# Performance work log

Measured on AMD Instinct MI355X. Metric: run time of the kernel, lower is better.

Reference implementation:

```python
import jax, jax.numpy as jnp
import numpy as np

T, B, I, H = 2048, 256, 512, 512


def setup_inputs() -> dict:
    key = jax.random.key(0)
    ks = jax.random.split(key, 7)
    s = 1.0 / np.sqrt(H).astype(np.float32)
    x = jax.random.normal(ks[0], (T, B, I), dtype=jnp.float32)
    # PyTorch nn.LSTM parameter layout: gates stacked as [i, f, g, o], each HxI / HxH
    W_ih = jax.random.uniform(ks[1], (4 * H, I), jnp.float32, -s, s)
    W_hh = jax.random.uniform(ks[2], (4 * H, H), jnp.float32, -s, s)
    b_ih = jax.random.uniform(ks[3], (4 * H,), jnp.float32, -s, s)
    b_hh = jax.random.uniform(ks[4], (4 * H,), jnp.float32, -s, s)
    W_out = jax.random.uniform(ks[5], (1, H), jnp.float32, -s, s)
    b_out = jax.random.uniform(ks[6], (1,), jnp.float32, -s, s)
    return {"x": x, "W_ih": W_ih, "W_hh": W_hh, "b_ih": b_ih, "b_hh": b_hh,
            "W_out": W_out, "b_out": b_out, "future": 0}


def _lstm_outputs(x, W_ih, W_hh, b_ih, b_hh):
    # Precompute input contribution for all timesteps: [T, B, 4H]
    x_proj = jnp.einsum('tbi,gi->tbg', x, W_ih) + b_ih + b_hh
    h0 = jnp.zeros((x.shape[1], W_hh.shape[1]), dtype=x.dtype)
    c0 = jnp.zeros_like(h0)

    def step(carry, xp):
        h, c = carry
        gates = xp + h @ W_hh.T                      # [B, 4H]
        i, f, g, o = jnp.split(gates, 4, axis=-1)    # torch gate order i,f,g,o
        i = jax.nn.sigmoid(i)
        f = jax.nn.sigmoid(f)
        g = jnp.tanh(g)
        o = jax.nn.sigmoid(o)
        c = f * c + i * g
        h = o * jnp.tanh(c)
        return (h, c), h

    _, hs = jax.lax.scan(step, (h0, c0), x_proj)     # hs: [T, B, H]
    return hs


def reference(x, W_ih, W_hh, b_ih, b_hh, W_out, b_out, future):
    # future == 0 in the only runnable configuration of the original module.
    hs = _lstm_outputs(x, W_ih, W_hh, b_ih, b_hh)
    out = hs @ W_out.T + b_out                       # per-step Linear(H -> 1): [T, B, 1]
    return out
```

## Files before the change

### kernel.cpp

```cpp
#include <hip/hip_runtime.h>

#define T_STEPS 2048
#define BATCH   256
#define ISZ     512
#define HSZ     512
#define GSZ     2048
#define KSZ     1024
#define XH      1024

#define SWZ(row, col) ((col) ^ (((row) & 7) << 4))

using bf16x8 = __attribute__((ext_vector_type(8))) __bf16;
using f32x4  = __attribute__((ext_vector_type(4))) float;
using i32x4  = __attribute__((ext_vector_type(4))) int;


__device__ __forceinline__ unsigned short f2bf(float f) {
    unsigned int u = __float_as_uint(f);
    unsigned int r = (u + 0x7FFFu + ((u >> 16) & 1u)) >> 16;
    return (unsigned short)r;
}
__device__ __forceinline__ float bf2f(unsigned int bits16) {
    return __uint_as_float(bits16 << 16);
}
__device__ __forceinline__ float sigf(float x)   { return 1.0f / (1.0f + __expf(-x)); }
__device__ __forceinline__ float tanh_f(float x) { return 2.0f / (1.0f + __expf(-2.0f * x)) - 1.0f; }

__global__ void pack_weights(const float* __restrict__ Wih,
                             const float* __restrict__ Whh,
                             unsigned short* __restrict__ Wcat) {
    int gid = blockIdx.x * blockDim.x + threadIdx.x;
    int n   = gid >> 8;
    int k4  = (gid & 255) * 4;
    const float* src = (k4 < ISZ) ? (Wih + (size_t)n * ISZ + k4)
                                  : (Whh + (size_t)n * HSZ + (k4 - ISZ));
    float4 v = *(const float4*)src;
    ushort4 o;
    o.x = f2bf(v.x); o.y = f2bf(v.y); o.z = f2bf(v.z); o.w = f2bf(v.w);
    *(ushort4*)(Wcat + (size_t)n * KSZ + k4) = o;
}

__global__ void init_state(unsigned int* __restrict__ thbufs,
                           float* __restrict__ bias,
                           const float* __restrict__ b_ih, const float* __restrict__ b_hh) {
    int gid = blockIdx.x * blockDim.x + threadIdx.x;
    if (gid < 262144) thbufs[gid] = 0u;
    if (gid < GSZ)    bias[gid] = b_ih[gid] + b_hh[gid];
}

__global__ __launch_bounds__(512, 2) void lstm_persist(
    const float* __restrict__ x,
    const unsigned short* __restrict__ Wcat,
    const float* __restrict__ bias,
    const float* __restrict__ Wout,
    const float* __restrict__ bout,
    unsigned long long* thbuf0,
    unsigned long long* thbuf1,
    float* __restrict__ out)
{
    __shared__ __align__(16) char xlds0[16 * XH];
    __shared__ __align__(16) char xlds1[16 * XH];
    __shared__ __align__(16) char hlds [16 * XH];
    __shared__ float gbuf[4][16][35];
    __shared__ float obuf[4];

    const int tid  = threadIdx.x;
    const int lane = tid & 63;
    const int w    = tid >> 6;
    const int gate = w & 3;
    const bool isx = (w < 4);
    const int g    = blockIdx.x & 15;
    const int wgi  = blockIdx.x >> 4;
    const int r0   = lane & 15;
    const int hi   = lane >> 4;

    const int kb = isx ? 0 : 16;
    const int n0 = gate * HSZ + wgi * 32 + r0;
    const int n1 = n0 + 16;
    bf16x8 wf0[16], wf1[16];
    #pragma unroll
    for (int it = 0; it < 16; ++it) {
        wf0[it] = *(const bf16x8*)(Wcat + (size_t)n0 * KSZ + (kb + it) * 32 + hi * 8);
        wf1[it] = *(const bf16x8*)(Wcat + (size_t)n1 * KSZ + (kb + it) * 32 + hi * 8);
    }
    #pragma unroll
    for (int it = 0; it < 16; ++it) {
        asm volatile("" : "+v"(wf0[it]));
        asm volatile("" : "+v"(wf1[it]));
    }
    const float bv0 = bias[n0];
    const float bv1 = bias[n1];
    const float bo  = bout[0];

    const int pr = tid >> 5;
    const int pc = tid & 31;
    float cst = 0.f;

    float woA = 0.f, woB = 0.f;
    if (isx) { woA = Wout[tid * 2]; woB = Wout[tid * 2 + 1]; }

    const int prow = (w - 4) * 4 + hi;
    const unsigned long long tb0 = (unsigned long long)thbuf0;
    const unsigned long long tb1 = (unsigned long long)thbuf1;
    const unsigned long long poff =
        ((unsigned long long)(g * 16 + (isx ? 0 : prow)) * 256) * 8 + (unsigned)(r0 * 16);
    const unsigned long long soff =
        ((unsigned long long)(g * 16 + pr) * 256 + wgi * 16 + (pc >> 1)) * 8;

    const int xorv = (r0 & 7) << 4;

    float4 xr[8];
    const int xrow = w * 4 + hi;
    const int xwoff = SWZ(xrow, r0 * 8);

    if (isx) {
        const float* xb = x + ((size_t)(g * 16 + xrow)) * ISZ + r0 * 4;
        #pragma unroll
        for (int s = 0; s < 8; ++s) xr[s] = *(const float4*)(xb + s * 64);
        #pragma unroll
        for (int s = 0; s < 8; ++s) {
            float4 v = xr[s];
            ushort4 o;
            o.x = f2bf(v.x); o.y = f2bf(v.y); o.z = f2bf(v.z); o.w = f2bf(v.w);
            *(ushort4*)(xlds0 + xrow * XH + xwoff + s * 128) = o;
        }
        const float* xb1 = x + ((size_t)BATCH + g * 16 + xrow) * ISZ + r0 * 4;
        #pragma unroll
        for (int s = 0; s < 8; ++s) xr[s] = *(const float4*)(xb1 + s * 64);
    }
    __syncthreads();

    #pragma unroll 1
    for (int t = 0; ; ++t) {
        if (isx) {
            if (t < T_STEPS) {
                f32x4 a0a = {0.f,0.f,0.f,0.f}, a0b = {0.f,0.f,0.f,0.f};
                f32x4 a1a = {0.f,0.f,0.f,0.f}, a1b = {0.f,0.f,0.f,0.f};
                const char* xsrc = ((t & 1) ? xlds1 : xlds0) + r0 * XH;
                #pragma unroll
                for (int it = 0; it < 16; it += 2) {
                    bf16x8 ae = *(const bf16x8*)(xsrc + ((hi * 16 + it * 64) ^ xorv));
                    bf16x8 ao = *(const bf16x8*)(xsrc + ((hi * 16 + (it + 1) * 64) ^ xorv));
                    a0a = __builtin_amdgcn_mfma_f32_16x16x32_bf16(ae, wf0[it],   a0a, 0, 0, 0);
                    a1a = __builtin_amdgcn_mfma_f32_16x16x32_bf16(ae, wf1[it],   a1a, 0, 0, 0);
                    a0b = __builtin_amdgcn_mfma_f32_16x16x32_bf16(ao, wf0[it+1], a0b, 0, 0, 0);
                    a1b = __builtin_amdgcn_mfma_f32_16x16x32_bf16(ao, wf1[it+1], a1b, 0, 0, 0);
                }
                #pragma unroll
                for (int j = 0; j < 4; ++j) {
                    gbuf[gate][hi * 4 + j][r0]      = a0a[j] + a0b[j] + bv0;
                    gbuf[gate][hi * 4 + j][16 + r0] = a1a[j] + a1b[j] + bv1;
                }
                if (t + 1 < T_STEPS) {
                    char* xd = (((t + 1) & 1) ? xlds1 : xlds0) + xrow * XH + xwoff;
                    #pragma unroll
                    for (int s = 0; s < 8; ++s) {
                        float4 v = xr[s];
                        ushort4 o;
                        o.x = f2bf(v.x); o.y = f2bf(v.y); o.z = f2bf(v.z); o.w = f2bf(v.w);
                        *(ushort4*)(xd + s * 128) = o;
                    }
                    int tp = (t + 2 < T_STEPS) ? t + 2 : T_STEPS - 1;
                    const float* xb = x + ((size_t)tp * BATCH + g * 16 + xrow) * ISZ + r0 * 4;
                    #pragma unroll
                    for (int s = 0; s < 8; ++s) xr[s] = *(const float4*)(xb + s * 64);
                }
            }
        } else {
            char* hd = hlds + prow * XH + (SWZ(prow, r0 * 8));
            if (t == 0) {
                #pragma unroll
                for (int s = 0; s < 8; ++s)
                    *(unsigned long long*)(hd + s * 128) = 0ull;
            } else {
                const unsigned long long psrc = (((t - 1) & 1) ? tb1 : tb0) + poff;
                const int tgt = t;
                i32x4 q0, q1, q2, q3, q4, q5, q6, q7;
                while (true) {
                    asm volatile(
                        "global_load_dwordx4 %0, %8, off sc0 sc1\n\t"
                        "global_load_dwordx4 %1, %8, off offset:256 sc0 sc1\n\t"
                        "global_load_dwordx4 %2, %8, off offset:512 sc0 sc1\n\t"
                        "global_load_dwordx4 %3, %8, off offset:768 sc0 sc1\n\t"
                        "global_load_dwordx4 %4, %8, off offset:1024 sc0 sc1\n\t"
                        "global_load_dwordx4 %5, %8, off offset:1280 sc0 sc1\n\t"
                        "global_load_dwordx4 %6, %8, off offset:1536 sc0 sc1\n\t"
                        "global_load_dwordx4 %7, %8, off offset:1792 sc0 sc1\n\t"
                        "s_waitcnt vmcnt(0)"
                        : "=&v"(q0), "=&v"(q1), "=&v"(q2), "=&v"(q3),
                          "=&v"(q4), "=&v"(q5), "=&v"(q6), "=&v"(q7)
                        : "v"(psrc) : "memory");
                    bool ok = (q0[1] >= tgt) & (q0[3] >= tgt) & (q1[1] >= tgt) & (q1[3] >= tgt)
                            & (q2[1] >= tgt) & (q2[3] >= tgt) & (q3[1] >= tgt) & (q3[3] >= tgt)
                            & (q4[1] >= tgt) & (q4[3] >= tgt) & (q5[1] >= tgt) & (q5[3] >= tgt)
                            & (q6[1] >= tgt) & (q6[3] >= tgt) & (q7[1] >= tgt) & (q7[3] >= tgt);
                    if (__all((int)ok)) {
                        *(unsigned long long*)(hd +   0) = (unsigned long long)(unsigned)q0[0] | ((unsigned long long)(unsigned)q0[2] << 32);
                        *(unsigned long long*)(hd + 128) = (unsigned long long)(unsigned)q1[0] | ((unsigned long long)(unsigned)q1[2] << 32);
                        *(unsigned long long*)(hd + 256) = (unsigned long long)(unsigned)q2[0] | ((unsigned long long)(unsigned)q2[2] << 32);
                        *(unsigned long long*)(hd + 384) = (unsigned long long)(unsigned)q3[0] | ((unsigned long long)(unsigned)q3[2] << 32);
                        *(unsigned long long*)(hd + 512) = (unsigned long long)(unsigned)q4[0] | ((unsigned long long)(unsigned)q4[2] << 32);
                        *(unsigned long long*)(hd + 640) = (unsigned long long)(unsigned)q5[0] | ((unsigned long long)(unsigned)q5[2] << 32);
                        *(unsigned long long*)(hd + 768) = (unsigned long long)(unsigned)q6[0] | ((unsigned long long)(unsigned)q6[2] << 32);
                        *(unsigned long long*)(hd + 896) = (unsigned long long)(unsigned)q7[0] | ((unsigned long long)(unsigned)q7[2] << 32);
                        break;
                    }
                }
            }
        }
        __syncthreads();

        if (isx) {
            if (t > 0) {
                unsigned pw2 = *(const unsigned*)(hlds + wgi * XH + (SWZ(wgi, tid * 4)));
                float ps = woA * bf2f(pw2 & 0xffffu) + woB * bf2f(pw2 >> 16);
                ps += __shfl_xor(ps, 1);
                ps += __shfl_xor(ps, 2);
                ps += __shfl_xor(ps, 4);
                ps += __shfl_xor(ps, 8);
                ps += __shfl_xor(ps, 16);
                ps += __shfl_xor(ps, 32);
                if (lane == 0) obuf[w] = ps;
            }
        } else if (t < T_STEPS) {
            f32x4 a0a = {0.f,0.f,0.f,0.f}, a0b = {0.f,0.f,0.f,0.f};
            f32x4 a1a = {0.f,0.f,0.f,0.f}, a1b = {0.f,0.f,0.f,0.f};
            const char* hsrc = hlds + r0 * XH;
            #pragma unroll
            for (int it = 0; it < 16; it += 2) {
                bf16x8 ae = *(const bf16x8*)(hsrc + ((hi * 16 + it * 64) ^ xorv));
                bf16x8 ao = *(const bf16x8*)(hsrc + ((hi * 16 + (it + 1) * 64) ^ xorv));
                a0a = __builtin_amdgcn_mfma_f32_16x16x32_bf16(ae, wf0[it],   a0a, 0, 0, 0);
                a1a = __builtin_amdgcn_mfma_f32_16x16x32_bf16(ae, wf1[it],   a1a, 0, 0, 0);
                a0b = __builtin_amdgcn_mfma_f32_16x16x32_bf16(ao, wf0[it+1], a0b, 0, 0, 0);
                a1b = __builtin_amdgcn_mfma_f32_16x16x32_bf16(ao, wf1[it+1], a1b, 0, 0, 0);
            }
            #pragma unroll
            for (int j = 0; j < 4; ++j) {
                gbuf[gate][hi * 4 + j][r0]      += a0a[j] + a0b[j];
                gbuf[gate][hi * 4 + j][16 + r0] += a1a[j] + a1b[j];
            }
        }
        __syncthreads();

        if (t > 0 && tid == 0)
            out[(size_t)(t - 1) * BATCH + g * 16 + wgi] =
                obuf[0] + obuf[1] + obuf[2] + obuf[3] + bo;
        if (t == T_STEPS) break;

        {
            float iv = sigf(gbuf[0][pr][pc]);
            float fv = sigf(gbuf[1][pr][pc]);
            float gv = tanh_f(gbuf[2][pr][pc]);
            float ov = sigf(gbuf[3][pr][pc]);
            cst = fv * cst + iv * gv;
            float hval = ov * tanh_f(cst);
            unsigned hb16 = (unsigned)f2bf(hval);
            unsigned partner = __shfl_xor(hb16, 1);
            if (!(tid & 1)) {
                unsigned hv2 = hb16 | (partner << 16);
                unsigned long long word = (unsigned long long)hv2
                                        | ((unsigned long long)(unsigned)(t + 1) << 32);
                unsigned long long dst = ((t & 1) ? tb1 : tb0) + soff;
                asm volatile("global_store_dwordx2 %0, %1, off sc0 sc1\n\t"
                             "s_waitcnt vmcnt(0)"
                             :: "v"(dst), "v"(word) : "memory");
            }
        }
        __syncthreads();
    }
}

extern "C" void kernel_launch(void* const* d_in, const int* in_sizes, int n_in,
                              void* d_out, int out_size, void* d_ws, size_t ws_size,
                              hipStream_t stream) {
    const float* x    = (const float*)d_in[0];
    const float* Wih  = (const float*)d_in[1];
    const float* Whh  = (const float*)d_in[2];
    const float* bih  = (const float*)d_in[3];
    const float* bhh  = (const float*)d_in[4];
    const float* Wout = (const float*)d_in[5];
    const float* bout = (const float*)d_in[6];

    char* ws = (char*)d_ws;
    unsigned short*     Wcat = (unsigned short*)(ws);
    float*              bias = (float*)(ws + 4194304);
    unsigned long long* th0  = (unsigned long long*)(ws + 4202496);
    unsigned long long* th1  = (unsigned long long*)(ws + 4726784);
    float*              out  = (float*)d_out;

    pack_weights<<<2048, 256, 0, stream>>>(Wih, Whh, Wcat);
    init_state<<<2048, 256, 0, stream>>>((unsigned int*)th0, bias, bih, bhh);
    lstm_persist<<<256, 512, 0, stream>>>(x, Wcat, bias, Wout, bout, th0, th1, out);
}
```

Before: 5.164 ms.

## Move gate pointwise to MFMA waves, drop store wait, use lightweight barriers

The LSTM pointwise update now runs only on the four h-waves, each thread computing two adjacent hidden units, so the partner shuffle is gone. The global publish store no longer waits on vmcnt(0); a dummy asm use of the published word keeps it live until the next poll loop. __syncthreads is replaced by an explicit lgkmcnt wait plus s_barrier, which does not wait on outstanding global memory ops. Resident weight fragments are pinned to AGPRs instead of VGPRs to relieve VGPR pressure. The aim is to shorten the serial per-step critical path, at the risk of weaker memory-ordering guarantees on the cross-block flag store.

```diff
diff --git a/kernel.cpp b/kernel.cpp
--- a/kernel.cpp
+++ b/kernel.cpp
@@ -13,6 +13,8 @@
 using bf16x8 = __attribute__((ext_vector_type(8))) __bf16;
 using f32x4  = __attribute__((ext_vector_type(4))) float;
 using i32x4  = __attribute__((ext_vector_type(4))) int;
+
+#define BARL() asm volatile("s_waitcnt lgkmcnt(0)\n\ts_barrier" ::: "memory")
 
 
 __device__ __forceinline__ unsigned short f2bf(float f) {
@@ -85,16 +87,17 @@
     }
     #pragma unroll
     for (int it = 0; it < 16; ++it) {
-        asm volatile("" : "+v"(wf0[it]));
-        asm volatile("" : "+v"(wf1[it]));
+        asm volatile("" : "+a"(wf0[it]));
+        asm volatile("" : "+a"(wf1[it]));
     }
     const float bv0 = bias[n0];
     const float bv1 = bias[n1];
     const float bo  = bout[0];
 
-    const int pr = tid >> 5;
-    const int pc = tid & 31;
-    float cst = 0.f;
+    const int ht  = tid & 255;
+    const int pr2 = ht >> 4;
+    const int cl  = (ht & 15) * 2;
+    float cst0 = 0.f, cst1 = 0.f;
 
     float woA = 0.f, woB = 0.f;
     if (isx) { woA = Wout[tid * 2]; woB = Wout[tid * 2 + 1]; }
@@ -105,7 +108,8 @@
     const unsigned long long poff =
         ((unsigned long long)(g * 16 + (isx ? 0 : prow)) * 256) * 8 + (unsigned)(r0 * 16);
     const unsigned long long soff =
-        ((unsigned long long)(g * 16 + pr) * 256 + wgi * 16 + (pc >> 1)) * 8;
+        ((unsigned long long)(g * 16 + pr2) * 256 + wgi * 16 + (ht & 15)) * 8;
+    unsigned long long pubword = 0ull;
 
     const int xorv = (r0 & 7) << 4;
 
@@ -206,9 +210,10 @@
                         break;
                     }
                 }
-            }
-        }
-        __syncthreads();
+                asm volatile("" :: "v"(pubword));
+            }
+        }
+        BARL();
 
         if (isx) {
             if (t > 0) {
@@ -241,33 +246,30 @@
                 gbuf[gate][hi * 4 + j][16 + r0] += a1a[j] + a1b[j];
             }
         }
-        __syncthreads();
+        BARL();
 
         if (t > 0 && tid == 0)
             out[(size_t)(t - 1) * BATCH + g * 16 + wgi] =
                 obuf[0] + obuf[1] + obuf[2] + obuf[3] + bo;
         if (t == T_STEPS) break;
 
-        {
-            float iv = sigf(gbuf[0][pr][pc]);
-            float fv = sigf(gbuf[1][pr][pc]);
-            float gv = tanh_f(gbuf[2][pr][pc]);
-            float ov = sigf(gbuf[3][pr][pc]);
-            cst = fv * cst + iv * gv;
-            float hval = ov * tanh_f(cst);
-            unsigned hb16 = (unsigned)f2bf(hval);
-            unsigned partner = __shfl_xor(hb16, 1);
-            if (!(tid & 1)) {
-                unsigned hv2 = hb16 | (partner << 16);
-                unsigned long long word = (unsigned long long)hv2
-                                        | ((unsigned long long)(unsigned)(t + 1) << 32);
-                unsigned long long dst = ((t & 1) ? tb1 : tb0) + soff;
-                asm volatile("global_store_dwordx2 %0, %1, off sc0 sc1\n\t"
-                             "s_waitcnt vmcnt(0)"
-                             :: "v"(dst), "v"(word) : "memory");
-            }
-        }
-        __syncthreads();
+        if (!isx) {
+            float iv0 = sigf(gbuf[0][pr2][cl]),     iv1 = sigf(gbuf[0][pr2][cl + 1]);
+            float fv0 = sigf(gbuf[1][pr2][cl]),     fv1 = sigf(gbuf[1][pr2][cl + 1]);
+            float gv0 = tanh_f(gbuf[2][pr2][cl]),   gv1 = tanh_f(gbuf[2][pr2][cl + 1]);
+            float ov0 = sigf(gbuf[3][pr2][cl]),     ov1 = sigf(gbuf[3][pr2][cl + 1]);
+            cst0 = fv0 * cst0 + iv0 * gv0;
+            cst1 = fv1 * cst1 + iv1 * gv1;
+            float h0f = ov0 * tanh_f(cst0);
+            float h1f = ov1 * tanh_f(cst1);
+            unsigned hv2 = (unsigned)f2bf(h0f) | ((unsigned)f2bf(h1f) << 16);
+            pubword = (unsigned long long)hv2
+                    | ((unsigned long long)(unsigned)(t + 1) << 32);
+            unsigned long long dst = ((t & 1) ? tb1 : tb0) + soff;
+            asm volatile("global_store_dwordx2 %0, %1, off sc0 sc1"
+                         :: "v"(dst), "v"(pubword) : "memory");
+        }
+        BARL();
     }
 }
 
```

Measured after the change: 6.030 ms. +16.8%, slower.

## Split each gate's column tile across two wave halves with 1024-thread blocks

Applied to the files above, without the earlier changes.

Doubles the block size from 512 to 1024 threads. Each wave now computes one 16-column half of its gate tile instead of both halves, which halves the MFMA chain and weight registers per wave. The x staging, h polling loads and activation/state update are redistributed over the extra waves, with the cell update and h publish moved to the h-side waves only. This aims to shorten the serial per-step critical path through more parallelism, at the cost of more threads taking part in each block barrier and different LDS and global access patterns for the h polling.

```diff
diff --git a/kernel.cpp b/kernel.cpp
--- a/kernel.cpp
+++ b/kernel.cpp
@@ -48,7 +48,7 @@
     if (gid < GSZ)    bias[gid] = b_ih[gid] + b_hh[gid];
 }
 
-__global__ __launch_bounds__(512, 2) void lstm_persist(
+__global__ __launch_bounds__(1024, 4) void lstm_persist(
     const float* __restrict__ x,
     const unsigned short* __restrict__ Wcat,
     const float* __restrict__ bias,
@@ -68,65 +68,60 @@
     const int lane = tid & 63;
     const int w    = tid >> 6;
     const int gate = w & 3;
-    const bool isx = (w < 4);
+    const int khalf = (w >> 2) & 1;
+    const int colhalf = w >> 3;
+    const bool isx = (khalf == 0);
     const int g    = blockIdx.x & 15;
     const int wgi  = blockIdx.x >> 4;
     const int r0   = lane & 15;
     const int hi   = lane >> 4;
 
-    const int kb = isx ? 0 : 16;
-    const int n0 = gate * HSZ + wgi * 32 + r0;
-    const int n1 = n0 + 16;
-    bf16x8 wf0[16], wf1[16];
+    const int u = (colhalf << 8) | (gate << 6) | lane;
+
+    const int n0 = gate * HSZ + wgi * 32 + colhalf * 16 + r0;
+    const int kb = khalf * 16;
+    bf16x8 wf[16];
     #pragma unroll
-    for (int it = 0; it < 16; ++it) {
-        wf0[it] = *(const bf16x8*)(Wcat + (size_t)n0 * KSZ + (kb + it) * 32 + hi * 8);
-        wf1[it] = *(const bf16x8*)(Wcat + (size_t)n1 * KSZ + (kb + it) * 32 + hi * 8);
-    }
-    #pragma unroll
-    for (int it = 0; it < 16; ++it) {
-        asm volatile("" : "+v"(wf0[it]));
-        asm volatile("" : "+v"(wf1[it]));
-    }
+    for (int it = 0; it < 16; ++it)
+        wf[it] = *(const bf16x8*)(Wcat + (size_t)n0 * KSZ + (kb + it) * 32 + hi * 8);
     const float bv0 = bias[n0];
-    const float bv1 = bias[n1];
     const float bo  = bout[0];
 
-    const int pr = tid >> 5;
-    const int pc = tid & 31;
+    const int pr = u >> 5;
+    const int pc = u & 31;
     float cst = 0.f;
 
     float woA = 0.f, woB = 0.f;
-    if (isx) { woA = Wout[tid * 2]; woB = Wout[tid * 2 + 1]; }
-
-    const int prow = (w - 4) * 4 + hi;
+    if (tid < 256) { woA = Wout[tid * 2]; woB = Wout[tid * 2 + 1]; }
+
     const unsigned long long tb0 = (unsigned long long)thbuf0;
     const unsigned long long tb1 = (unsigned long long)thbuf1;
     const unsigned long long poff =
-        ((unsigned long long)(g * 16 + (isx ? 0 : prow)) * 256) * 8 + (unsigned)(r0 * 16);
+        ((unsigned long long)(g * 16 + pr) * 256) * 8 + (unsigned)(pc * 64);
     const unsigned long long soff =
         ((unsigned long long)(g * 16 + pr) * 256 + wgi * 16 + (pc >> 1)) * 8;
 
     const int xorv = (r0 & 7) << 4;
 
-    float4 xr[8];
-    const int xrow = w * 4 + hi;
-    const int xwoff = SWZ(xrow, r0 * 8);
+    float4 xr[4];
+    const int xrow = u >> 5;
+    const int xc16 = u & 31;
 
     if (isx) {
-        const float* xb = x + ((size_t)(g * 16 + xrow)) * ISZ + r0 * 4;
+        const float* xb = x + ((size_t)(g * 16 + xrow)) * ISZ + xc16 * 16;
         #pragma unroll
-        for (int s = 0; s < 8; ++s) xr[s] = *(const float4*)(xb + s * 64);
+        for (int s = 0; s < 4; ++s) xr[s] = *(const float4*)(xb + s * 4);
+        char* xd = xlds0 + xrow * XH;
         #pragma unroll
-        for (int s = 0; s < 8; ++s) {
+        for (int s = 0; s < 4; ++s) {
             float4 v = xr[s];
             ushort4 o;
             o.x = f2bf(v.x); o.y = f2bf(v.y); o.z = f2bf(v.z); o.w = f2bf(v.w);
-            *(ushort4*)(xlds0 + xrow * XH + xwoff + s * 128) = o;
-        }
-        const float* xb1 = x + ((size_t)BATCH + g * 16 + xrow) * ISZ + r0 * 4;
+            *(ushort4*)(xd + SWZ(xrow, xc16 * 32 + s * 8)) = o;
+        }
+        const float* xb1 = x + ((size_t)BATCH + g * 16 + xrow) * ISZ + xc16 * 16;
         #pragma unroll
-        for (int s = 0; s < 8; ++s) xr[s] = *(const float4*)(xb1 + s * 64);
+        for (int s = 0; s < 4; ++s) xr[s] = *(const float4*)(xb1 + s * 4);
     }
     __syncthreads();
 
@@ -134,75 +129,63 @@
     for (int t = 0; ; ++t) {
         if (isx) {
             if (t < T_STEPS) {
-                f32x4 a0a = {0.f,0.f,0.f,0.f}, a0b = {0.f,0.f,0.f,0.f};
-                f32x4 a1a = {0.f,0.f,0.f,0.f}, a1b = {0.f,0.f,0.f,0.f};
+                f32x4 aa = {0.f,0.f,0.f,0.f}, ab = {0.f,0.f,0.f,0.f};
                 const char* xsrc = ((t & 1) ? xlds1 : xlds0) + r0 * XH;
                 #pragma unroll
                 for (int it = 0; it < 16; it += 2) {
                     bf16x8 ae = *(const bf16x8*)(xsrc + ((hi * 16 + it * 64) ^ xorv));
                     bf16x8 ao = *(const bf16x8*)(xsrc + ((hi * 16 + (it + 1) * 64) ^ xorv));
-                    a0a = __builtin_amdgcn_mfma_f32_16x16x32_bf16(ae, wf0[it],   a0a, 0, 0, 0);
-                    a1a = __builtin_amdgcn_mfma_f32_16x16x32_bf16(ae, wf1[it],   a1a, 0, 0, 0);
-                    a0b = __builtin_amdgcn_mfma_f32_16x16x32_bf16(ao, wf0[it+1], a0b, 0, 0, 0);
-                    a1b = __builtin_amdgcn_mfma_f32_16x16x32_bf16(ao, wf1[it+1], a1b, 0, 0, 0);
+                    aa = __builtin_amdgcn_mfma_f32_16x16x32_bf16(ae, wf[it],     aa, 0, 0, 0);
+                    ab = __builtin_amdgcn_mfma_f32_16x16x32_bf16(ao, wf[it + 1], ab, 0, 0, 0);
                 }
                 #pragma unroll
-                for (int j = 0; j < 4; ++j) {
-                    gbuf[gate][hi * 4 + j][r0]      = a0a[j] + a0b[j] + bv0;
-                    gbuf[gate][hi * 4 + j][16 + r0] = a1a[j] + a1b[j] + bv1;
-                }
+                for (int j = 0; j < 4; ++j)
+                    gbuf[gate][hi * 4 + j][colhalf * 16 + r0] = aa[j] + ab[j] + bv0;
                 if (t + 1 < T_STEPS) {
-                    char* xd = (((t + 1) & 1) ? xlds1 : xlds0) + xrow * XH + xwoff;
+                    char* xd = (((t + 1) & 1) ? xlds1 : xlds0) + xrow * XH;
                     #pragma unroll
-                    for (int s = 0; s < 8; ++s) {
+                    for (int s = 0; s < 4; ++s) {
                         float4 v = xr[s];
                         ushort4 o;
                         o.x = f2bf(v.x); o.y = f2bf(v.y); o.z = f2bf(v.z); o.w = f2bf(v.w);
-                        *(ushort4*)(xd + s * 128) = o;
+                        *(ushort4*)(xd + SWZ(xrow, xc16 * 32 + s * 8)) = o;
                     }
                     int tp = (t + 2 < T_STEPS) ? t + 2 : T_STEPS - 1;
-                    const float* xb = x + ((size_t)tp * BATCH + g * 16 + xrow) * ISZ + r0 * 4;
+                    const float* xb = x + ((size_t)tp * BATCH + g * 16 + xrow) * ISZ + xc16 * 16;
                     #pragma unroll
-                    for (int s = 0; s < 8; ++s) xr[s] = *(const float4*)(xb + s * 64);
+                    for (int s = 0; s < 4; ++s) xr[s] = *(const float4*)(xb + s * 4);
                 }
             }
         } else {
-            char* hd = hlds + prow * XH + (SWZ(prow, r0 * 8));
+            char* hd = hlds + pr * XH;
             if (t == 0) {
                 #pragma unroll
-                for (int s = 0; s < 8; ++s)
-                    *(unsigned long long*)(hd + s * 128) = 0ull;
+                for (int s = 0; s < 4; ++s)
+                    *(unsigned long long*)(hd + SWZ(pr, pc * 32 + s * 8)) = 0ull;
             } else {
                 const unsigned long long psrc = (((t - 1) & 1) ? tb1 : tb0) + poff;
                 const int tgt = t;
-                i32x4 q0, q1, q2, q3, q4, q5, q6, q7;
+                i32x4 q0, q1, q2, q3;
                 while (true) {
                     asm volatile(
-                        "global_load_dwordx4 %0, %8, off sc0 sc1\n\t"
-                        "global_load_dwordx4 %1, %8, off offset:256 sc0 sc1\n\t"
-                        "global_load_dwordx4 %2, %8, off offset:512 sc0 sc1\n\t"
-                        "global_load_dwordx4 %3, %8, off offset:768 sc0 sc1\n\t"
-                        "global_load_dwordx4 %4, %8, off offset:1024 sc0 sc1\n\t"
-                        "global_load_dwordx4 %5, %8, off offset:1280 sc0 sc1\n\t"
-                        "global_load_dwordx4 %6, %8, off offset:1536 sc0 sc1\n\t"
-                        "global_load_dwordx4 %7, %8, off offset:1792 sc0 sc1\n\t"
+                        "global_load_dwordx4 %0, %4, off sc0 sc1\n\t"
+                        "global_load_dwordx4 %1, %4, off offset:16 sc0 sc1\n\t"
+                        "global_load_dwordx4 %2, %4, off offset:32 sc0 sc1\n\t"
+                        "global_load_dwordx4 %3, %4, off offset:48 sc0 sc1\n\t"
                         "s_waitcnt vmcnt(0)"
-                        : "=&v"(q0), "=&v"(q1), "=&v"(q2), "=&v"(q3),
-                          "=&v"(q4), "=&v"(q5), "=&v"(q6), "=&v"(q7)
+                        : "=&v"(q0), "=&v"(q1), "=&v"(q2), "=&v"(q3)
                         : "v"(psrc) : "memory");
                     bool ok = (q0[1] >= tgt) & (q0[3] >= tgt) & (q1[1] >= tgt) & (q1[3] >= tgt)
-                            & (q2[1] >= tgt) & (q2[3] >= tgt) & (q3[1] >= tgt) & (q3[3] >= tgt)
-                            & (q4[1] >= tgt) & (q4[3] >= tgt) & (q5[1] >= tgt) & (q5[3] >= tgt)
-                            & (q6[1] >= tgt) & (q6[3] >= tgt) & (q7[1] >= tgt) & (q7[3] >= tgt);
+                            & (q2[1] >= tgt) & (q2[3] >= tgt) & (q3[1] >= tgt) & (q3[3] >= tgt);
                     if (__all((int)ok)) {
-                        *(unsigned long long*)(hd +   0) = (unsigned long long)(unsigned)q0[0] | ((unsigned long long)(unsigned)q0[2] << 32);
-                        *(unsigned long long*)(hd + 128) = (unsigned long long)(unsigned)q1[0] | ((unsigned long long)(unsigned)q1[2] << 32);
-                        *(unsigned long long*)(hd + 256) = (unsigned long long)(unsigned)q2[0] | ((unsigned long long)(unsigned)q2[2] << 32);
-                        *(unsigned long long*)(hd + 384) = (unsigned long long)(unsigned)q3[0] | ((unsigned long long)(unsigned)q3[2] << 32);
-                        *(unsigned long long*)(hd + 512) = (unsigned long long)(unsigned)q4[0] | ((unsigned long long)(unsigned)q4[2] << 32);
-                        *(unsigned long long*)(hd + 640) = (unsigned long long)(unsigned)q5[0] | ((unsigned long long)(unsigned)q5[2] << 32);
-                        *(unsigned long long*)(hd + 768) = (unsigned long long)(unsigned)q6[0] | ((unsigned long long)(unsigned)q6[2] << 32);
-                        *(unsigned long long*)(hd + 896) = (unsigned long long)(unsigned)q7[0] | ((unsigned long long)(unsigned)q7[2] << 32);
+                        *(unsigned long long*)(hd + SWZ(pr, pc * 32 +  0)) =
+                            (unsigned long long)(unsigned)q0[0] | ((unsigned long long)(unsigned)q0[2] << 32);
+                        *(unsigned long long*)(hd + SWZ(pr, pc * 32 +  8)) =
+                            (unsigned long long)(unsigned)q1[0] | ((unsigned long long)(unsigned)q1[2] << 32);
+                        *(unsigned long long*)(hd + SWZ(pr, pc * 32 + 16)) =
+                            (unsigned long long)(unsigned)q2[0] | ((unsigned long long)(unsigned)q2[2] << 32);
+                        *(unsigned long long*)(hd + SWZ(pr, pc * 32 + 24)) =
+                            (unsigned long long)(unsigned)q3[0] | ((unsigned long long)(unsigned)q3[2] << 32);
                         break;
                     }
                 }
@@ -211,7 +194,7 @@
         __syncthreads();
 
         if (isx) {
-            if (t > 0) {
+            if (t > 0 && tid < 256) {
                 unsigned pw2 = *(const unsigned*)(hlds + wgi * XH + (SWZ(wgi, tid * 4)));
                 float ps = woA * bf2f(pw2 & 0xffffu) + woB * bf2f(pw2 >> 16);
                 ps += __shfl_xor(ps, 1);
@@ -223,23 +206,18 @@
                 if (lane == 0) obuf[w] = ps;
             }
         } else if (t < T_STEPS) {
-            f32x4 a0a = {0.f,0.f,0.f,0.f}, a0b = {0.f,0.f,0.f,0.f};
-            f32x4 a1a = {0.f,0.f,0.f,0.f}, a1b = {0.f,0.f,0.f,0.f};
+            f32x4 aa = {0.f,0.f,0.f,0.f}, ab = {0.f,0.f,0.f,0.f};
             const char* hsrc = hlds + r0 * XH;
             #pragma unroll
             for (int it = 0; it < 16; it += 2) {
                 bf16x8 ae = *(const bf16x8*)(hsrc + ((hi * 16 + it * 64) ^ xorv));
                 bf16x8 ao = *(const bf16x8*)(hsrc + ((hi * 16 + (it + 1) * 64) ^ xorv));
-                a0a = __builtin_amdgcn_mfma_f32_16x16x32_bf16(ae, wf0[it],   a0a, 0, 0, 0);
-                a1a = __builtin_amdgcn_mfma_f32_16x16x32_bf16(ae, wf1[it],   a1a, 0, 0, 0);
-                a0b = __builtin_amdgcn_mfma_f32_16x16x32_bf16(ao, wf0[it+1], a0b, 0, 0, 0);
-                a1b = __builtin_amdgcn_mfma_f32_16x16x32_bf16(ao, wf1[it+1], a1b, 0, 0, 0);
+                aa = __builtin_amdgcn_mfma_f32_16x16x32_bf16(ae, wf[it],     aa, 0, 0, 0);
+                ab = __builtin_amdgcn_mfma_f32_16x16x32_bf16(ao, wf[it + 1], ab, 0, 0, 0);
             }
             #pragma unroll
-            for (int j = 0; j < 4; ++j) {
-                gbuf[gate][hi * 4 + j][r0]      += a0a[j] + a0b[j];
-                gbuf[gate][hi * 4 + j][16 + r0] += a1a[j] + a1b[j];
-            }
+            for (int j = 0; j < 4; ++j)
+                gbuf[gate][hi * 4 + j][colhalf * 16 + r0] += aa[j] + ab[j];
         }
         __syncthreads();
 
@@ -248,7 +226,7 @@
                 obuf[0] + obuf[1] + obuf[2] + obuf[3] + bo;
         if (t == T_STEPS) break;
 
-        {
+        if (!isx) {
             float iv = sigf(gbuf[0][pr][pc]);
             float fv = sigf(gbuf[1][pr][pc]);
             float gv = tanh_f(gbuf[2][pr][pc]);
@@ -257,7 +235,7 @@
             float hval = ov * tanh_f(cst);
             unsigned hb16 = (unsigned)f2bf(hval);
             unsigned partner = __shfl_xor(hb16, 1);
-            if (!(tid & 1)) {
+            if (!(u & 1)) {
                 unsigned hv2 = hb16 | (partner << 16);
                 unsigned long long word = (unsigned long long)hv2
                                         | ((unsigned long long)(unsigned)(t + 1) << 32);
@@ -291,5 +269,5 @@
 
     pack_weights<<<2048, 256, 0, stream>>>(Wih, Whh, Wcat);
     init_state<<<2048, 256, 0, stream>>>((unsigned int*)th0, bias, bih, bhh);
-    lstm_persist<<<256, 512, 0, stream>>>(x, Wcat, bias, Wout, bout, th0, th1, out);
-}
+    lstm_persist<<<256, 1024, 0, stream>>>(x, Wcat, bias, Wout, bout, th0, th1, out);
+}
```

Measured after the change: 7.849 ms. 1.52x slower.
